# Performance work log

Hardware: AMD Instinct MI355X
Metric: run time of the kernel (lower is better)

The kernel has to match this reference:

```python
import jax, jax.numpy as jnp
import numpy as np

B, L, C, R = 4, 2048, 64, 8
A_SCALE = 0.1  # keeps spectral radius of per-step A < 1 so 2048-step products stay stable


def setup_inputs() -> dict:
    key = jax.random.key(0)
    k1, k2, k3, k4 = jax.random.split(key, 4)
    A_re = jax.random.normal(k1, (B, L, C, R, R), jnp.float32) * A_SCALE
    A_im = jax.random.normal(k2, (B, L, C, R, R), jnp.float32) * A_SCALE
    X_re = jax.random.normal(k3, (B, L, C, R), jnp.float32)
    X_im = jax.random.normal(k4, (B, L, C, R), jnp.float32)
    return {"A_re": A_re, "A_im": A_im, "X_re": X_re, "X_im": X_im}


def reference(A_re, A_im, X_re, X_im):
    # Complex linear recurrence: Y_t = A_t @ Y_{t-1} + X_t (Y_0 = X_0),
    # computed as a parallel associative scan over the L axis, matching
    # the Triton combine_fn: (a1,x1) o (a2,x2) = (a2@a1, a2@x1 + x2).
    A = jax.lax.complex(A_re, A_im)  # [B,L,C,R,R] complex64
    X = jax.lax.complex(X_re, X_im)  # [B,L,C,R]   complex64

    def combine(left, right):
        a1, x1 = left
        a2, x2 = right
        new_a = jnp.matmul(a2, a1)                          # [.,R,R]@[.,R,R]
        new_x = jnp.einsum('...ij,...j->...i', a2, x1) + x2  # [.,R,R]@[.,R]
        return (new_a, new_x)

    _, Y = jax.lax.associative_scan(combine, (A, X), axis=1)
    # Return real/imag stacked so the output dtype is float32: [B,L,C,R,2]
    return jnp.stack((jnp.real(Y), jnp.imag(Y)), axis=-1)
```

## Files before the change

### kernel.cpp

```cpp
#include <hip/hip_runtime.h>

#define B 4
#define L 2048
#define C 64
#define R 8
#define NCH (B * C)
#define TQ 16
#define S (L / TQ)
#define GRP (NCH / 8)


#define GLL(gp, lp, sz)                                                        \
    __builtin_amdgcn_global_load_lds(                                          \
        (const __attribute__((address_space(1))) void*)(gp),                   \
        (__attribute__((address_space(3))) void*)(lp), sz, 0, 0)

__global__ __launch_bounds__(256) void k_summary(
    const float* __restrict__ Are, const float* __restrict__ Aim,
    const float* __restrict__ Xre, const float* __restrict__ Xim,
    float2* __restrict__ sumP, float2* __restrict__ sumQ)
{
    __shared__ __align__(16) float sm[4 * 2 * 1152];
    const int lane = threadIdx.x & 63;
    const int w = __builtin_amdgcn_readfirstlane((int)(threadIdx.x >> 6));
    const int c = lane >> 3, r = lane & 7;
    const int s = blockIdx.x >> 3;
    const int g = (blockIdx.x & 7) * 4 + w;
    const int n0 = g * 8;
    const int b = n0 >> 6;
    const int cc0 = n0 & (C - 1);
    const int n = n0 + c;
    const int tbase = s * TQ;

    const int q = (lane >> 1) & 7, h = lane & 1;
    const int c0 = lane >> 4, c1 = 4 + (lane >> 4);
    const int o0 = c0 * 16 + ((q ^ c0) << 1) + h;
    const int o1 = c1 * 16 + ((q ^ c1) << 1) + h;

    char* lw = ((char*)sm) + w * 9216;
    const float* wb = sm + w * 2304;

    float Pre[8], Pim[8];
#pragma unroll
    for (int k = 0; k < 8; ++k) { Pre[k] = (k == r) ? 1.f : 0.f; Pim[k] = 0.f; }
    float qre = 0.f, qim = 0.f;

#define ISSUE1(t, bf)                                                          \
    {                                                                          \
        const int fb = (b * L + (t)) * C + cc0;                                \
        const float4* gA = (const float4*)(Are + (long)fb * 64);               \
        const float4* gI = (const float4*)(Aim + (long)fb * 64);               \
        char* lb = lw + (bf) * 4608;                                           \
        GLL(gA + o0, lb, 16);                                                  \
        GLL(gA + o1, lb + 1024, 16);                                           \
        GLL(gI + o0, lb + 2048, 16);                                           \
        GLL(gI + o1, lb + 3072, 16);                                           \
        GLL(Xre + (long)fb * 8 + lane, lb + 4096, 4);                          \
        GLL(Xim + (long)fb * 8 + lane, lb + 4352, 4);                          \
    }

#define COMPUTE_STEP1(bp)                                                      \
    {                                                                          \
        float xr[8], xi[8];                                                    \
        *(float4*)&xr[0] = *(const float4*)((bp) + 1024 + c * 8);              \
        *(float4*)&xr[4] = *(const float4*)((bp) + 1024 + c * 8 + 4);          \
        *(float4*)&xi[0] = *(const float4*)((bp) + 1088 + c * 8);              \
        *(float4*)&xi[4] = *(const float4*)((bp) + 1088 + c * 8 + 4);          \
        _Pragma("unroll")                                                      \
        for (int k = 0; k < 8; ++k) {                                          \
            qre += Pre[k] * xr[k] - Pim[k] * xi[k];                            \
            qim += Pre[k] * xi[k] + Pim[k] * xr[k];                            \
        }                                                                      \
        float Nre[8], Nim[8];                                                  \
        _Pragma("unroll")                                                      \
        for (int j = 0; j < 8; ++j) { Nre[j] = 0.f; Nim[j] = 0.f; }            \
        _Pragma("unroll")                                                      \
        for (int k = 0; k < 8; ++k) {                                          \
            const int ko = ((k ^ c) << 3);                                     \
            float er[8], ei[8];                                                \
            *(float4*)&er[0] = *(const float4*)((bp) + c * 64 + ko);           \
            *(float4*)&er[4] = *(const float4*)((bp) + c * 64 + ko + 4);       \
            *(float4*)&ei[0] = *(const float4*)((bp) + 512 + c * 64 + ko);     \
            *(float4*)&ei[4] = *(const float4*)((bp) + 512 + c * 64 + ko + 4); \
            const float pr = Pre[k], pi = Pim[k];                              \
            _Pragma("unroll")                                                  \
            for (int j = 0; j < 8; ++j) {                                      \
                Nre[j] += pr * er[j] - pi * ei[j];                             \
                Nim[j] += pr * ei[j] + pi * er[j];                             \
            }                                                                  \
        }                                                                      \
        _Pragma("unroll")                                                      \
        for (int k = 0; k < 8; ++k) { Pre[k] = Nre[k]; Pim[k] = Nim[k]; }      \
    }

    ISSUE1(tbase + TQ - 1, 0);
#pragma unroll 1
    for (int tt = 0; tt < TQ - 1; ++tt) {
        ISSUE1(tbase + TQ - 2 - tt, (tt + 1) & 1);
        asm volatile("s_waitcnt vmcnt(6)" ::: "memory");
        __builtin_amdgcn_sched_barrier(0);
        const float* bp = wb + (tt & 1) * 1152;
        COMPUTE_STEP1(bp);
    }
    asm volatile("s_waitcnt vmcnt(0)" ::: "memory");
    __builtin_amdgcn_sched_barrier(0);
    {
        const float* bp = wb + ((TQ - 1) & 1) * 1152;
        COMPUTE_STEP1(bp);
    }

    float4* gp = (float4*)(sumP + ((long)(s * 256 + n) * 8 + r) * 8);
    gp[0] = make_float4(Pre[0], Pim[0], Pre[1], Pim[1]);
    gp[1] = make_float4(Pre[2], Pim[2], Pre[3], Pim[3]);
    gp[2] = make_float4(Pre[4], Pim[4], Pre[5], Pim[5]);
    gp[3] = make_float4(Pre[6], Pim[6], Pre[7], Pim[7]);
    sumQ[(long)(s * 256 + n) * 8 + r] = make_float2(qre, qim);
}

__global__ __launch_bounds__(64) void k_carry(
    const float2* __restrict__ sumP, const float2* __restrict__ sumQ,
    float2* __restrict__ carry)
{
    const int lane = threadIdx.x;
    const int c = lane >> 3, r = lane & 7;
    const int n = blockIdx.x * 8 + c;

    float yr = 0.f, yi = 0.f;
    long base = (long)n * 8;
    const float4* prow0 = (const float4*)(sumP + (base + r) * 8);
    float4 p0 = prow0[0], p1 = prow0[1], p2 = prow0[2], p3 = prow0[3];
    float2 qv = sumQ[base + r];

#pragma unroll 1
    for (int s = 0; s < S; ++s) {
        carry[base + r] = make_float2(yr, yi);
        float yvr[8], yvi[8];
#pragma unroll
        for (int k = 0; k < 8; ++k) {
            yvr[k] = __shfl(yr, (c << 3) + k, 64);
            yvi[k] = __shfl(yi, (c << 3) + k, 64);
        }
        float4 w0 = p0, w1 = p1, w2 = p2, w3 = p3;
        float2 qq = qv;
        if (s + 1 < S) {
            const long nb = base + 2048;
            const float4* np = (const float4*)(sumP + (nb + r) * 8);
            p0 = np[0]; p1 = np[1]; p2 = np[2]; p3 = np[3];
            qv = sumQ[nb + r];
        }
        float prr[8], pri[8];
        prr[0]=w0.x; pri[0]=w0.y; prr[1]=w0.z; pri[1]=w0.w;
        prr[2]=w1.x; pri[2]=w1.y; prr[3]=w1.z; pri[3]=w1.w;
        prr[4]=w2.x; pri[4]=w2.y; prr[5]=w2.z; pri[5]=w2.w;
        prr[6]=w3.x; pri[6]=w3.y; prr[7]=w3.z; pri[7]=w3.w;
        float nr0 = qq.x, ni0 = qq.y, nr1 = 0.f, ni1 = 0.f;
#pragma unroll
        for (int k = 0; k < 8; k += 2) {
            nr0 += prr[k] * yvr[k] - pri[k] * yvi[k];
            ni0 += prr[k] * yvi[k] + pri[k] * yvr[k];
            nr1 += prr[k+1] * yvr[k+1] - pri[k+1] * yvi[k+1];
            ni1 += prr[k+1] * yvi[k+1] + pri[k+1] * yvr[k+1];
        }
        yr = nr0 + nr1; yi = ni0 + ni1;
        base += 2048;
    }
}

__global__ __launch_bounds__(256) void k_fixup(
    const float* __restrict__ Are, const float* __restrict__ Aim,
    const float* __restrict__ Xre, const float* __restrict__ Xim,
    const float2* __restrict__ carry, float2* __restrict__ out)
{
    const int lane = threadIdx.x & 63;
    const int w = threadIdx.x >> 6;
    const int c = lane >> 3, r = lane & 7;
    const int blk = (int)gridDim.x - 1 - (int)blockIdx.x;
    const int s = blk >> 3;
    const int g = (blk & 7) * 4 + w;
    const int n0 = g * 8;
    const int b = n0 >> 6;
    const int cc0 = n0 & (C - 1);
    const int n = n0 + c;
    const int tbase = s * TQ;

    float yvr[8], yvi[8];
    {
        const float4* cv = (const float4*)(carry + (long)(s * 256 + n) * 8);
        float4 w0 = cv[0], w1 = cv[1], w2 = cv[2], w3 = cv[3];
        yvr[0]=w0.x; yvi[0]=w0.y; yvr[1]=w0.z; yvi[1]=w0.w;
        yvr[2]=w1.x; yvi[2]=w1.y; yvr[3]=w1.z; yvi[3]=w1.w;
        yvr[4]=w2.x; yvi[4]=w2.y; yvr[5]=w2.z; yvi[5]=w2.w;
        yvr[6]=w3.x; yvi[6]=w3.y; yvr[7]=w3.z; yvi[7]=w3.w;
    }

    float4 sa0, sa1, si0, si1; float sxr, sxi;
    float4 ta0, ta1, ti0, ti1; float txr, txi;

#define LOADSET3(t, A0, A1, I0, I1, XR, XI)                                    \
    {                                                                          \
        const int fb = (b * L + (t)) * C + cc0;                                \
        const float4* pA = (const float4*)(Are + (long)fb * 64) + lane * 2;    \
        const float4* pI = (const float4*)(Aim + (long)fb * 64) + lane * 2;    \
        A0 = pA[0]; A1 = pA[1]; I0 = pI[0]; I1 = pI[1];                        \
        XR = Xre[(long)fb * 8 + lane]; XI = Xim[(long)fb * 8 + lane];          \
    }

#define FIX_STEP(A0, A1, I0, I1, XR_, XI_, t)                                  \
    {                                                                          \
        float nr0 = (XR_), ni0 = (XI_), nr1 = 0.f, ni1 = 0.f;                  \
        nr0 += A0.x * yvr[0] - I0.x * yvi[0];                                  \
        ni0 += A0.x * yvi[0] + I0.x * yvr[0];                                  \
        nr1 += A0.y * yvr[1] - I0.y * yvi[1];                                  \
        ni1 += A0.y * yvi[1] + I0.y * yvr[1];                                  \
        nr0 += A0.z * yvr[2] - I0.z * yvi[2];                                  \
        ni0 += A0.z * yvi[2] + I0.z * yvr[2];                                  \
        nr1 += A0.w * yvr[3] - I0.w * yvi[3];                                  \
        ni1 += A0.w * yvi[3] + I0.w * yvr[3];                                  \
        nr0 += A1.x * yvr[4] - I1.x * yvi[4];                                  \
        ni0 += A1.x * yvi[4] + I1.x * yvr[4];                                  \
        nr1 += A1.y * yvr[5] - I1.y * yvi[5];                                  \
        ni1 += A1.y * yvi[5] + I1.y * yvr[5];                                  \
        nr0 += A1.z * yvr[6] - I1.z * yvi[6];                                  \
        ni0 += A1.z * yvi[6] + I1.z * yvr[6];                                  \
        nr1 += A1.w * yvr[7] - I1.w * yvi[7];                                  \
        ni1 += A1.w * yvi[7] + I1.w * yvr[7];                                  \
        const float nr = nr0 + nr1, ni = ni0 + ni1;                            \
        const int fb = (b * L + (t)) * C + cc0;                                \
        out[(long)fb * 8 + lane] = make_float2(nr, ni);                        \
        _Pragma("unroll")                                                      \
        for (int k = 0; k < 8; ++k) {                                          \
            yvr[k] = __shfl(nr, (c << 3) + k, 64);                             \
            yvi[k] = __shfl(ni, (c << 3) + k, 64);                             \
        }                                                                      \
    }

    LOADSET3(tbase + 0, sa0, sa1, si0, si1, sxr, sxi);
    LOADSET3(tbase + 1, ta0, ta1, ti0, ti1, txr, txi);

#pragma unroll 1
    for (int tt = 0; tt < TQ; tt += 2) {
        float4 A0 = sa0, A1 = sa1, I0 = si0, I1 = si1;
        float XR = sxr, XI = sxi;
        if (tt + 2 < TQ) LOADSET3(tbase + tt + 2, sa0, sa1, si0, si1, sxr, sxi);
        FIX_STEP(A0, A1, I0, I1, XR, XI, tbase + tt);
        float4 B0 = ta0, B1 = ta1, J0 = ti0, J1 = ti1;
        float YR = txr, YI = txi;
        if (tt + 3 < TQ) LOADSET3(tbase + tt + 3, ta0, ta1, ti0, ti1, txr, txi);
        FIX_STEP(B0, B1, J0, J1, YR, YI, tbase + tt + 1);
    }
}

extern "C" void kernel_launch(void* const* d_in, const int* in_sizes, int n_in,
                              void* d_out, int out_size, void* d_ws, size_t ws_size,
                              hipStream_t stream)
{
    const float* Are = (const float*)d_in[0];
    const float* Aim = (const float*)d_in[1];
    const float* Xre = (const float*)d_in[2];
    const float* Xim = (const float*)d_in[3];
    float2* out = (float2*)d_out;

    float2* sumP  = (float2*)d_ws;
    float2* sumQ  = sumP + (long)S * NCH * 64;
    float2* carry = sumQ + (long)S * NCH * 8;

    k_summary<<<(S * GRP) / 4, 256, 0, stream>>>(Are, Aim, Xre, Xim, sumP, sumQ);
    k_carry<<<NCH / 8, 64, 0, stream>>>(sumP, sumQ, carry);
    k_fixup<<<(S * GRP) / 4, 256, 0, stream>>>(Are, Aim, Xre, Xim, carry, out);
}
```

Baseline: 456.2 us.

## Replace LDS-direct loads with register-staged double buffering and deepen carry prefetch

In the summary kernel, the global_load_lds async copies are replaced by ordinary coalesced float4 global loads into registers. These are then written to a padded LDS layout, and loads for two steps ahead stay in flight while the current step computes. The carry kernel now prefetches four scan segments ahead instead of one, to hide global-load latency on its serial chain. The cost is more registers and extra LDS write instructions, and the summary kernel has no explicit barrier between LDS writes and reads within a wave.

```diff
diff --git a/kernel.cpp b/kernel.cpp
--- a/kernel.cpp
+++ b/kernel.cpp
@@ -10,17 +10,12 @@
 #define GRP (NCH / 8)
 
 
-#define GLL(gp, lp, sz)                                                        \
-    __builtin_amdgcn_global_load_lds(                                          \
-        (const __attribute__((address_space(1))) void*)(gp),                   \
-        (__attribute__((address_space(3))) void*)(lp), sz, 0, 0)
-
 __global__ __launch_bounds__(256) void k_summary(
     const float* __restrict__ Are, const float* __restrict__ Aim,
     const float* __restrict__ Xre, const float* __restrict__ Xim,
     float2* __restrict__ sumP, float2* __restrict__ sumQ)
 {
-    __shared__ __align__(16) float sm[4 * 2 * 1152];
+    __shared__ __align__(16) float sm[4 * 2 * 1248];
     const int lane = threadIdx.x & 63;
     const int w = __builtin_amdgcn_readfirstlane((int)(threadIdx.x >> 6));
     const int c = lane >> 3, r = lane & 7;
@@ -32,81 +27,85 @@
     const int n = n0 + c;
     const int tbase = s * TQ;
 
-    const int q = (lane >> 1) & 7, h = lane & 1;
-    const int c0 = lane >> 4, c1 = 4 + (lane >> 4);
-    const int o0 = c0 * 16 + ((q ^ c0) << 1) + h;
-    const int o1 = c1 * 16 + ((q ^ c1) << 1) + h;
-
-    char* lw = ((char*)sm) + w * 9216;
-    const float* wb = sm + w * 2304;
-
-    float Pre[8], Pim[8];
+    char* const smw = ((char*)sm) + w * 9984;
+    char* const wrA = smw + 272 * c + 32 * r;
+    char* const wrX = smw + 4352 + 80 * c + 4 * r;
+    const char* const rdA = smw + 272 * c;
+    const char* const rdX = smw + 4352 + 80 * c;
+
+    const int fb0 = (b * L + (tbase + TQ - 1)) * C + cc0;
+    const float* pA  = Are + (long)fb0 * 64 + lane * 8;
+    const float* pI  = Aim + (long)fb0 * 64 + lane * 8;
+    const float* pXr = Xre + (long)fb0 * 8 + lane;
+    const float* pXi = Xim + (long)fb0 * 8 + lane;
+
+    float Pre[8], Pim[8], Nre[8], Nim[8];
 #pragma unroll
     for (int k = 0; k < 8; ++k) { Pre[k] = (k == r) ? 1.f : 0.f; Pim[k] = 0.f; }
     float qre = 0.f, qim = 0.f;
 
-#define ISSUE1(t, bf)                                                          \
-    {                                                                          \
-        const int fb = (b * L + (t)) * C + cc0;                                \
-        const float4* gA = (const float4*)(Are + (long)fb * 64);               \
-        const float4* gI = (const float4*)(Aim + (long)fb * 64);               \
-        char* lb = lw + (bf) * 4608;                                           \
-        GLL(gA + o0, lb, 16);                                                  \
-        GLL(gA + o1, lb + 1024, 16);                                           \
-        GLL(gI + o0, lb + 2048, 16);                                           \
-        GLL(gI + o1, lb + 3072, 16);                                           \
-        GLL(Xre + (long)fb * 8 + lane, lb + 4096, 4);                          \
-        GLL(Xim + (long)fb * 8 + lane, lb + 4352, 4);                          \
-    }
-
-#define COMPUTE_STEP1(bp)                                                      \
+    float4 sa0, sa1, si0, si1; float sxr, sxi;
+    float4 ta0, ta1, ti0, ti1; float txr, txi;
+
+#define SLOAD(A0, A1, I0, I1, XR, XI)                                          \
+    {                                                                          \
+        A0 = *(const float4*)pA; A1 = *(const float4*)(pA + 4);                \
+        I0 = *(const float4*)pI; I1 = *(const float4*)(pI + 4);                \
+        XR = *pXr; XI = *pXi;                                                  \
+        pA -= 4096; pI -= 4096; pXr -= 512; pXi -= 512;                        \
+    }
+
+#define SSTAGE(BUF, A0, A1, I0, I1, XR, XI)                                    \
+    {                                                                          \
+        *(float4*)(wrA + (BUF)) = A0;                                          \
+        *(float4*)(wrA + (BUF) + 16) = A1;                                     \
+        *(float4*)(wrA + (BUF) + 2176) = I0;                                   \
+        *(float4*)(wrA + (BUF) + 2176 + 16) = I1;                              \
+        *(float*)(wrX + (BUF)) = XR;                                           \
+        *(float*)(wrX + (BUF) + 32) = XI;                                      \
+    }
+
+#define SCOMP(BUF, SRe, SIm, DRe, DIm)                                         \
     {                                                                          \
         float xr[8], xi[8];                                                    \
-        *(float4*)&xr[0] = *(const float4*)((bp) + 1024 + c * 8);              \
-        *(float4*)&xr[4] = *(const float4*)((bp) + 1024 + c * 8 + 4);          \
-        *(float4*)&xi[0] = *(const float4*)((bp) + 1088 + c * 8);              \
-        *(float4*)&xi[4] = *(const float4*)((bp) + 1088 + c * 8 + 4);          \
-        _Pragma("unroll")                                                      \
-        for (int k = 0; k < 8; ++k) {                                          \
-            qre += Pre[k] * xr[k] - Pim[k] * xi[k];                            \
-            qim += Pre[k] * xi[k] + Pim[k] * xr[k];                            \
-        }                                                                      \
-        float Nre[8], Nim[8];                                                  \
-        _Pragma("unroll")                                                      \
-        for (int j = 0; j < 8; ++j) { Nre[j] = 0.f; Nim[j] = 0.f; }            \
-        _Pragma("unroll")                                                      \
-        for (int k = 0; k < 8; ++k) {                                          \
-            const int ko = ((k ^ c) << 3);                                     \
+        *(float4*)&xr[0] = *(const float4*)(rdX + (BUF));                      \
+        *(float4*)&xr[4] = *(const float4*)(rdX + (BUF) + 16);                 \
+        *(float4*)&xi[0] = *(const float4*)(rdX + (BUF) + 32);                 \
+        *(float4*)&xi[4] = *(const float4*)(rdX + (BUF) + 48);                 \
+        _Pragma("unroll")                                                      \
+        for (int k = 0; k < 8; ++k) {                                          \
+            qre += SRe[k] * xr[k] - SIm[k] * xi[k];                            \
+            qim += SRe[k] * xi[k] + SIm[k] * xr[k];                            \
+        }                                                                      \
+        _Pragma("unroll")                                                      \
+        for (int j = 0; j < 8; ++j) { DRe[j] = 0.f; DIm[j] = 0.f; }            \
+        _Pragma("unroll")                                                      \
+        for (int k = 0; k < 8; ++k) {                                          \
             float er[8], ei[8];                                                \
-            *(float4*)&er[0] = *(const float4*)((bp) + c * 64 + ko);           \
-            *(float4*)&er[4] = *(const float4*)((bp) + c * 64 + ko + 4);       \
-            *(float4*)&ei[0] = *(const float4*)((bp) + 512 + c * 64 + ko);     \
-            *(float4*)&ei[4] = *(const float4*)((bp) + 512 + c * 64 + ko + 4); \
-            const float pr = Pre[k], pi = Pim[k];                              \
+            *(float4*)&er[0] = *(const float4*)(rdA + (BUF) + 32 * k);         \
+            *(float4*)&er[4] = *(const float4*)(rdA + (BUF) + 32 * k + 16);    \
+            *(float4*)&ei[0] = *(const float4*)(rdA + (BUF) + 2176 + 32 * k);  \
+            *(float4*)&ei[4] = *(const float4*)(rdA + (BUF) + 2192 + 32 * k);  \
+            const float pr = SRe[k], pi = SIm[k];                              \
             _Pragma("unroll")                                                  \
             for (int j = 0; j < 8; ++j) {                                      \
-                Nre[j] += pr * er[j] - pi * ei[j];                             \
-                Nim[j] += pr * ei[j] + pi * er[j];                             \
+                DRe[j] += pr * er[j] - pi * ei[j];                             \
+                DIm[j] += pr * ei[j] + pi * er[j];                             \
             }                                                                  \
         }                                                                      \
-        _Pragma("unroll")                                                      \
-        for (int k = 0; k < 8; ++k) { Pre[k] = Nre[k]; Pim[k] = Nim[k]; }      \
-    }
-
-    ISSUE1(tbase + TQ - 1, 0);
+    }
+
+    SLOAD(sa0, sa1, si0, si1, sxr, sxi);
+    SLOAD(ta0, ta1, ti0, ti1, txr, txi);
+
 #pragma unroll 1
-    for (int tt = 0; tt < TQ - 1; ++tt) {
-        ISSUE1(tbase + TQ - 2 - tt, (tt + 1) & 1);
-        asm volatile("s_waitcnt vmcnt(6)" ::: "memory");
-        __builtin_amdgcn_sched_barrier(0);
-        const float* bp = wb + (tt & 1) * 1152;
-        COMPUTE_STEP1(bp);
-    }
-    asm volatile("s_waitcnt vmcnt(0)" ::: "memory");
-    __builtin_amdgcn_sched_barrier(0);
-    {
-        const float* bp = wb + ((TQ - 1) & 1) * 1152;
-        COMPUTE_STEP1(bp);
+    for (int tt = TQ - 1; tt >= 1; tt -= 2) {
+        SSTAGE(0, sa0, sa1, si0, si1, sxr, sxi);
+        if (tt >= 3) SLOAD(sa0, sa1, si0, si1, sxr, sxi);
+        SCOMP(0, Pre, Pim, Nre, Nim);
+        SSTAGE(4992, ta0, ta1, ti0, ti1, txr, txi);
+        if (tt >= 3) SLOAD(ta0, ta1, ti0, ti1, txr, txi);
+        SCOMP(4992, Nre, Nim, Pre, Pim);
     }
 
     float4* gp = (float4*)(sumP + ((long)(s * 256 + n) * 8 + r) * 8);
@@ -124,45 +123,59 @@
     const int lane = threadIdx.x;
     const int c = lane >> 3, r = lane & 7;
     const int n = blockIdx.x * 8 + c;
+    const long base2 = (long)n * 8;
 
     float yr = 0.f, yi = 0.f;
-    long base = (long)n * 8;
-    const float4* prow0 = (const float4*)(sumP + (base + r) * 8);
-    float4 p0 = prow0[0], p1 = prow0[1], p2 = prow0[2], p3 = prow0[3];
-    float2 qv = sumQ[base + r];
+
+    float4 A0,A1,A2,A3, B0,B1,B2,B3, C0,C1,C2,C3, D0,D1,D2,D3;
+    float2 Aq, Bq, Cq, Dq;
+
+#define CLOAD(P0,P1,P2,P3,QV,SS)                                               \
+    {                                                                          \
+        const float4* np = (const float4*)(sumP + (base2 + (long)(SS) * 2048 + r) * 8); \
+        P0 = np[0]; P1 = np[1]; P2 = np[2]; P3 = np[3];                        \
+        QV = sumQ[base2 + (long)(SS) * 2048 + r];                              \
+    }
+
+#define CSTEP(P0,P1,P2,P3,QV,SS)                                               \
+    {                                                                          \
+        carry[base2 + (long)(SS) * 2048 + r] = make_float2(yr, yi);            \
+        float4 w0 = P0, w1 = P1, w2 = P2, w3 = P3;                             \
+        float2 qs = QV;                                                        \
+        if ((SS) + 4 < S) CLOAD(P0,P1,P2,P3,QV,(SS) + 4);                      \
+        float yvr[8], yvi[8];                                                  \
+        _Pragma("unroll")                                                      \
+        for (int k = 0; k < 8; ++k) {                                          \
+            yvr[k] = __shfl(yr, (c << 3) + k, 64);                             \
+            yvi[k] = __shfl(yi, (c << 3) + k, 64);                             \
+        }                                                                      \
+        float prr[8], pri[8];                                                  \
+        prr[0]=w0.x; pri[0]=w0.y; prr[1]=w0.z; pri[1]=w0.w;                    \
+        prr[2]=w1.x; pri[2]=w1.y; prr[3]=w1.z; pri[3]=w1.w;                    \
+        prr[4]=w2.x; pri[4]=w2.y; prr[5]=w2.z; pri[5]=w2.w;                    \
+        prr[6]=w3.x; pri[6]=w3.y; prr[7]=w3.z; pri[7]=w3.w;                    \
+        float nr0 = qs.x, ni0 = qs.y, nr1 = 0.f, ni1 = 0.f;                    \
+        _Pragma("unroll")                                                      \
+        for (int k = 0; k < 8; k += 2) {                                       \
+            nr0 += prr[k] * yvr[k] - pri[k] * yvi[k];                          \
+            ni0 += prr[k] * yvi[k] + pri[k] * yvr[k];                          \
+            nr1 += prr[k+1] * yvr[k+1] - pri[k+1] * yvi[k+1];                  \
+            ni1 += prr[k+1] * yvi[k+1] + pri[k+1] * yvr[k+1];                  \
+        }                                                                      \
+        yr = nr0 + nr1; yi = ni0 + ni1;                                        \
+    }
+
+    CLOAD(A0,A1,A2,A3,Aq, 0);
+    CLOAD(B0,B1,B2,B3,Bq, 1);
+    CLOAD(C0,C1,C2,C3,Cq, 2);
+    CLOAD(D0,D1,D2,D3,Dq, 3);
 
 #pragma unroll 1
-    for (int s = 0; s < S; ++s) {
-        carry[base + r] = make_float2(yr, yi);
-        float yvr[8], yvi[8];
-#pragma unroll
-        for (int k = 0; k < 8; ++k) {
-            yvr[k] = __shfl(yr, (c << 3) + k, 64);
-            yvi[k] = __shfl(yi, (c << 3) + k, 64);
-        }
-        float4 w0 = p0, w1 = p1, w2 = p2, w3 = p3;
-        float2 qq = qv;
-        if (s + 1 < S) {
-            const long nb = base + 2048;
-            const float4* np = (const float4*)(sumP + (nb + r) * 8);
-            p0 = np[0]; p1 = np[1]; p2 = np[2]; p3 = np[3];
-            qv = sumQ[nb + r];
-        }
-        float prr[8], pri[8];
-        prr[0]=w0.x; pri[0]=w0.y; prr[1]=w0.z; pri[1]=w0.w;
-        prr[2]=w1.x; pri[2]=w1.y; prr[3]=w1.z; pri[3]=w1.w;
-        prr[4]=w2.x; pri[4]=w2.y; prr[5]=w2.z; pri[5]=w2.w;
-        prr[6]=w3.x; pri[6]=w3.y; prr[7]=w3.z; pri[7]=w3.w;
-        float nr0 = qq.x, ni0 = qq.y, nr1 = 0.f, ni1 = 0.f;
-#pragma unroll
-        for (int k = 0; k < 8; k += 2) {
-            nr0 += prr[k] * yvr[k] - pri[k] * yvi[k];
-            ni0 += prr[k] * yvi[k] + pri[k] * yvr[k];
-            nr1 += prr[k+1] * yvr[k+1] - pri[k+1] * yvi[k+1];
-            ni1 += prr[k+1] * yvi[k+1] + pri[k+1] * yvr[k+1];
-        }
-        yr = nr0 + nr1; yi = ni0 + ni1;
-        base += 2048;
+    for (int ss = 0; ss < S; ss += 4) {
+        CSTEP(A0,A1,A2,A3,Aq, ss);
+        CSTEP(B0,B1,B2,B3,Bq, ss + 1);
+        CSTEP(C0,C1,C2,C3,Cq, ss + 2);
+        CSTEP(D0,D1,D2,D3,Dq, ss + 3);
     }
 }
 
```

New measurement: 409.9 us. 10.1% less time.
